# Kernel optimization log

Hardware: AMD Instinct MI355X
Metric: run time of the kernel (lower is better)

## Reference

```python
import jax, jax.numpy as jnp
import numpy as np

H = 256   # hidden_size
V = 47    # vocab
T = 257   # target sequence length (T-1 decode steps)
S = 1024  # encoder frames


def setup_inputs() -> dict:
    key = jax.random.key(0)
    ks = jax.random.split(key, 32)
    sc = 0.05
    n = lambda k, sh: jax.random.normal(k, sh, dtype=jnp.float32) * sc
    inp = {
        "Y": jax.random.randint(ks[0], (T,), 0, V),
        "h": n(ks[1], (3, 1, H)),
        "c": n(ks[2], (3, 1, H)),
        "outEncoder": n(ks[3], (S, H)),
        "emb": n(ks[4], (V, H)),
    }
    i = 5
    for l in (1, 2, 3):
        inp[f"W_ih{l}"] = n(ks[i], (4 * H, H)); i += 1
        inp[f"W_hh{l}"] = n(ks[i], (4 * H, H)); i += 1
        inp[f"b_ih{l}"] = n(ks[i], (4 * H,)); i += 1
        inp[f"b_hh{l}"] = n(ks[i], (4 * H,)); i += 1
    inp["att_vector"] = n(ks[i], (1, H)); i += 1
    inp["att_W"] = n(ks[i], (H, H)); i += 1
    inp["att_V"] = n(ks[i], (H, H)); i += 1
    inp["att_b"] = n(ks[i], (H, 1)); i += 1
    inp["mlp_w1"] = n(ks[i], (H, 2 * H)); i += 1
    inp["mlp_b1"] = n(ks[i], (H,)); i += 1
    inp["mlp_w2"] = n(ks[i], (H, H)); i += 1
    inp["mlp_b2"] = n(ks[i], (H,)); i += 1
    inp["mlp_w3"] = n(ks[i], (V, H)); i += 1
    inp["mlp_b3"] = n(ks[i], (V,)); i += 1
    inp["teacher_force"] = 0  # rand() > 0 always -> always teacher-forced (deterministic)
    return inp


def _lstm_cell(x, h, c, W_ih, W_hh, b_ih, b_hh):
    # PyTorch LSTMCell: gate order i, f, g, o
    g = x @ W_ih.T + b_ih + h @ W_hh.T + b_hh        # [1, 4H]
    i, f, gg, o = jnp.split(g, 4, axis=-1)
    c_new = jax.nn.sigmoid(f) * c + jax.nn.sigmoid(i) * jnp.tanh(gg)
    h_new = jax.nn.sigmoid(o) * jnp.tanh(c_new)
    return h_new, c_new


def reference(Y, h, c, outEncoder, emb,
              W_ih1, W_hh1, b_ih1, b_hh1,
              W_ih2, W_hh2, b_ih2, b_hh2,
              W_ih3, W_hh3, b_ih3, b_hh3,
              att_vector, att_W, att_V, att_b,
              mlp_w1, mlp_b1, mlp_w2, mlp_b2, mlp_w3, mlp_b3,
              teacher_force):
    # teacher_force == 0 -> ground-truth inputs every step (the only deterministic path)
    VOut = att_V @ outEncoder.T                      # [H, S], loop-invariant

    def step(carry, x):
        h0, c0, h1, c1, h2, c2 = carry
        h0, c0 = _lstm_cell(x, h0, c0, W_ih1, W_hh1, b_ih1, b_hh1)
        h1, c1 = _lstm_cell(h0, h1, c1, W_ih2, W_hh2, b_ih2, b_hh2)
        h2, c2 = _lstm_cell(h1, h2, c2, W_ih3, W_hh3, b_ih3, b_hh3)
        # Bahdanau-style attention: E = tanh(W h + V enc + b)
        WS = att_W @ h2.T                            # [H, 1] -> broadcasts over S
        E = jnp.tanh(WS + VOut + att_b)              # [H, S]
        e = att_vector @ E                           # [1, S]
        alpha = jax.nn.softmax(e, axis=1)            # [1, S]
        context = alpha @ outEncoder                 # [1, H]
        v = jnp.concatenate([h2, context], axis=1)   # [1, 2H]
        v = jax.nn.relu(v @ mlp_w1.T + mlp_b1)
        v = jax.nn.relu(v @ mlp_w2.T + mlp_b2)
        out = v @ mlp_w3.T + mlp_b3                  # [1, V]
        return (h0, c0, h1, c1, h2, c2), out

    xs = emb[Y[:-1]][:, None, :]                     # [T-1, 1, H] embedded teacher inputs
    init = (h[0], c[0], h[1], c[1], h[2], c[2])
    _, outs = jax.lax.scan(step, init, xs)
    return outs                                      # [T-1, 1, V]
```

## Files before the change

### kernel.cpp

```cpp
#include <hip/hip_runtime.h>


#define VOCAB  47
#define NSTEP  256
#define NREC   40
#define NTAIL  216
#define NMEGA  (NREC + NTAIL)

typedef unsigned long long u64;

#define F_H0A 64
#define F_H1A (F_H0A + 131584)
#define F_H2A (F_H1A + 131584)
#define F_X1  (F_H2A + 131584)
#define F_VB  (F_X1 + 262144)
#define F_W1T (F_VB + 262144)
#define F_W2T (F_W1T + 131072)
#define F_W3T (F_W2T + 65536)
#define F_AWT (F_W3T + 12032)

#define R_SHH 0
#define R_SHX 512
#define T_H2  0
#define T_WS  256
#define T_WSP 512
#define T_EX  1024
#define T_CAT 2048
#define T_O1  2560
#define T_O2  2816
#define T_AV  3072
#define T_RED 3328

__device__ __forceinline__ float fma4(float4 w, float4 h, float acc) {
    acc = fmaf(w.x, h.x, acc); acc = fmaf(w.y, h.y, acc);
    acc = fmaf(w.z, h.z, acc); acc = fmaf(w.w, h.w, acc);
    return acc;
}
__device__ __forceinline__ float sigm(float x) {
    return __builtin_amdgcn_rcpf(1.f + __expf(-x));
}
__device__ __forceinline__ float tanh_(float x) {
    float e = __expf(2.f * x);
    return 1.f - 2.f * __builtin_amdgcn_rcpf(e + 1.f);
}

__device__ __forceinline__ void tagstore(u64* p, float v, unsigned tag) {
    u64 pk = ((u64)tag << 32) | (u64)__float_as_uint(v);
    __hip_atomic_store(p, pk, __ATOMIC_RELAXED, __HIP_MEMORY_SCOPE_AGENT);
}
__device__ __forceinline__ float pollval(u64* p, unsigned tag) {
    u64 v;
    do { v = __hip_atomic_load(p, __ATOMIC_RELAXED, __HIP_MEMORY_SCOPE_AGENT); }
    while ((unsigned)(v >> 32) != tag);
    return __uint_as_float((unsigned)(v & 0xffffffffull));
}
__device__ __forceinline__ float pollval_slow(u64* p, unsigned tag) {
    u64 v;
    for (;;) {
        v = __hip_atomic_load(p, __ATOMIC_RELAXED, __HIP_MEMORY_SCOPE_AGENT);
        if ((unsigned)(v >> 32) == tag) break;
        __builtin_amdgcn_s_sleep(2);
    }
    return __uint_as_float((unsigned)(v & 0xffffffffull));
}

__global__ __launch_bounds__(256) void prep_kernel(
    const float* __restrict__ emb, const int* __restrict__ Y,
    const float* __restrict__ Wih1, const float* __restrict__ bih1,
    const float* __restrict__ bhh1,
    const float* __restrict__ enc, const float* __restrict__ attV,
    const float* __restrict__ attB,
    const float* __restrict__ w1, const float* __restrict__ w2,
    const float* __restrict__ w3, const float* __restrict__ attW,
    const float* __restrict__ h, float* __restrict__ wsf)
{
    __shared__ __align__(16) float psm[4160];
    const int id = blockIdx.x, tid = threadIdx.x;

    if (id < 512) {
        const float* Arows; const int* idx; const float* Brows;
        const float* bias1; const float* bias2; float* out; int C, rt, ct;
        if (id < 256) {
            Arows = emb; idx = Y; Brows = Wih1; bias1 = bih1; bias2 = bhh1;
            out = wsf + F_X1; C = 1024; rt = id & 15; ct = id >> 4;
        } else {
            Arows = enc; idx = nullptr; Brows = attV; bias1 = attB; bias2 = nullptr;
            out = wsf + F_VB; C = 256; rt = (id - 256) & 63; ct = (id - 256) >> 6;
        }
        float* sA = psm;
        const int rl = tid >> 4, l = tid & 15;
        const int r = rt * 16 + rl;
        const int cb = ct * 64;
        const int arow = idx ? idx[r] : r;
        const float* Ap = Arows + arow * 256;
#pragma unroll
        for (int q = 0; q < 4; ++q)
            *(float4*)(&sA[rl * 260 + l * 16 + 4 * q]) = *(const float4*)(Ap + l * 16 + 4 * q);
        __syncthreads();
        for (int cc = 0; cc < 64; ++cc) {
            const int c = cb + cc;
            const float* Bp = Brows + c * 256;
            float acc = 0.f;
#pragma unroll
            for (int q = 0; q < 4; ++q) {
                float4 b = *(const float4*)(Bp + l * 4 + 64 * q);
                float4 a = *(const float4*)(&sA[rl * 260 + l * 4 + 64 * q]);
                acc = fma4(b, a, acc);
            }
            acc += __shfl_xor(acc, 1); acc += __shfl_xor(acc, 2);
            acc += __shfl_xor(acc, 4); acc += __shfl_xor(acc, 8);
            if (l == 0) {
                float bb = bias1[c] + (bias2 ? bias2[c] : 0.f);
                out[(size_t)r * C + c] = acc + bb;
            }
        }
    } else if (id < 784) {
        const float* in; float* out; int rows, cols, bxi, byi;
        if (id < 640)      { in = w1;   out = wsf + F_W1T; rows = 256; cols = 512;
                             bxi = (id - 512) & 15; byi = (id - 512) >> 4; }
        else if (id < 704) { in = w2;   out = wsf + F_W2T; rows = 256; cols = 256;
                             bxi = (id - 640) & 7;  byi = (id - 640) >> 3; }
        else if (id < 720) { in = w3;   out = wsf + F_W3T; rows = VOCAB; cols = 256;
                             bxi = (id - 704) & 7;  byi = (id - 704) >> 3; }
        else               { in = attW; out = wsf + F_AWT; rows = 256; cols = 256;
                             bxi = (id - 720) & 7;  byi = (id - 720) >> 3; }
        float* tile = psm;
        const int tx = tid & 31, ty = tid >> 5;
        const int bx = bxi * 32, by = byi * 32;
        int x = bx + tx;
#pragma unroll
        for (int j = ty; j < 32; j += 8) {
            int y = by + j;
            if (x < cols && y < rows) tile[j * 33 + tx] = in[y * cols + x];
        }
        __syncthreads();
        x = by + tx;
#pragma unroll
        for (int j = ty; j < 32; j += 8) {
            int y = bx + j;
            if (x < rows && y < cols) out[y * rows + x] = tile[tx * 33 + j];
        }
    } else {
        tagstore((u64*)(wsf + F_H0A) + tid, h[tid],       1u);
        tagstore((u64*)(wsf + F_H1A) + tid, h[256 + tid], 1u);
        tagstore((u64*)(wsf + F_H2A) + tid, h[512 + tid], 1u);
    }
}

__global__ __launch_bounds__(512) void mega_kernel(
    const float* __restrict__ Whh1,
    const float* __restrict__ Wih2, const float* __restrict__ Whh2,
    const float* __restrict__ Wih3, const float* __restrict__ Whh3,
    const float* __restrict__ bih2, const float* __restrict__ bhh2,
    const float* __restrict__ bih3, const float* __restrict__ bhh3,
    const float* __restrict__ cin,  const float* __restrict__ av,
    const float* __restrict__ enc,
    const float* __restrict__ b1, const float* __restrict__ b2,
    const float* __restrict__ b3,
    float* __restrict__ wsf, float* __restrict__ out)
{
    __shared__ __align__(16) float smem[3456];
    const int tid = threadIdx.x, wg = blockIdx.x;
    const int wave = tid >> 6, wlane = tid & 63;

    u64* H0A = (u64*)(wsf + F_H0A);
    u64* H1A = (u64*)(wsf + F_H1A);
    u64* H2A = (u64*)(wsf + F_H2A);

    if (wg < 8) {
        const float* X1 = wsf + F_X1;
        const int ug = wlane >> 4, gate = (wlane >> 2) & 3, l4 = wlane & 3;
        const int u = wg * 32 + wave * 4 + ug;
        const int ju = gate * 256 + u;
        float4 wA[16];
        const float* wp = Whh1 + ju * 256;
#pragma unroll
        for (int m = 0; m < 16; ++m) wA[m] = *(const float4*)(wp + (m * 4 + l4) * 4);
        float creg = ((wlane & 15) == 0) ? cin[u] : 0.f;
        const int b16 = wlane & 48;

        float xv = (l4 == 0) ? X1[ju] : 0.f;
        for (int t = 0; t < NSTEP; ++t) {
            if (tid < 256)
                smem[R_SHH + (t & 1) * 256 + tid] = pollval(H0A + t * 256 + tid, t + 1);
            __syncthreads();
            const float4* a4 = (const float4*)(smem + R_SHH + (t & 1) * 256);
            float acc = xv;
#pragma unroll
            for (int m = 0; m < 16; ++m) acc = fma4(wA[m], a4[m * 4 + l4], acc);
            acc += __shfl_xor(acc, 1); acc += __shfl_xor(acc, 2);
            float gf = __shfl(acc, b16 + 4);
            float gg = __shfl(acc, b16 + 8);
            float go = __shfl(acc, b16 + 12);
            if ((wlane & 15) == 0) {
                float cn = sigm(gf) * creg + sigm(acc) * tanh_(gg);
                creg = cn;
                tagstore(H0A + (t + 1) * 256 + u, sigm(go) * tanh_(cn), t + 2);
            }
            if (t < NSTEP - 1) xv = (l4 == 0) ? X1[(t + 1) * 1024 + ju] : 0.f;
        }
    } else if (wg < NREC) {
        const int role = (wg < 24) ? 1 : 2;
        const int ug = wlane >> 5, gate = (wlane >> 3) & 3, l8 = wlane & 7;
        const int wgr = wg - (role == 1 ? 8 : 24);
        const int u = wgr * 16 + wave * 2 + ug;
        const int ju = gate * 256 + u;
        const float* Wi = (role == 1) ? Wih2 : Wih3;
        const float* Wh = (role == 1) ? Whh2 : Whh3;
        float4 wAi[8], wAh[8];
        const float* wip = Wi + ju * 256;
        const float* whp = Wh + ju * 256;
#pragma unroll
        for (int m = 0; m < 8; ++m) {
            wAi[m] = *(const float4*)(wip + (m * 8 + l8) * 4);
            wAh[m] = *(const float4*)(whp + (m * 8 + l8) * 4);
        }
        float biasr = (l8 == 0)
            ? ((role == 1) ? (bih2[ju] + bhh2[ju]) : (bih3[ju] + bhh3[ju])) : 0.f;
        float creg = ((wlane & 31) == 0) ? cin[((role == 1) ? 256 : 512) + u] : 0.f;
        u64* Hup  = (role == 1) ? H0A : H1A;
        u64* Hown = (role == 1) ? H1A : H2A;
        const int b32 = wlane & 32;

        if (tid < 256) smem[R_SHX + tid] = pollval(Hup + 256 + tid, 2);
        __syncthreads();
        float xacc;
        {
            const float4* x4 = (const float4*)(smem + R_SHX);
            float a = 0.f;
#pragma unroll
            for (int m = 0; m < 8; ++m) a = fma4(wAi[m], x4[m * 8 + l8], a);
            xacc = a;
        }

        for (int t = 0; t < NSTEP; ++t) {
            if (tid < 256)
                smem[R_SHH + (t & 1) * 256 + tid] = pollval(Hown + t * 256 + tid, t + 1);
            __syncthreads();
            const float4* h4 = (const float4*)(smem + R_SHH + (t & 1) * 256);
            float acc = xacc + biasr;
#pragma unroll
            for (int m = 0; m < 8; ++m) acc = fma4(wAh[m], h4[m * 8 + l8], acc);
            acc += __shfl_xor(acc, 1); acc += __shfl_xor(acc, 2); acc += __shfl_xor(acc, 4);
            float gf = __shfl(acc, b32 + 8);
            float gg = __shfl(acc, b32 + 16);
            float go = __shfl(acc, b32 + 24);
            if ((wlane & 31) == 0) {
                float cn = sigm(gf) * creg + sigm(acc) * tanh_(gg);
                creg = cn;
                tagstore(Hown + (t + 1) * 256 + u, sigm(go) * tanh_(cn), t + 2);
            }
            if (t < NSTEP - 1) {
                if (tid < 256)
                    smem[R_SHX + ((t + 1) & 1) * 256 + tid] =
                        pollval(Hup + (t + 2) * 256 + tid, t + 3);
                __syncthreads();
                const float4* x4 = (const float4*)(smem + R_SHX + ((t + 1) & 1) * 256);
                float a = 0.f;
#pragma unroll
                for (int m = 0; m < 8; ++m) a = fma4(wAi[m], x4[m * 8 + l8], a);
                xacc = a;
            }
        }
    } else {
        const float* VB  = wsf + F_VB;
        const float* W1T = wsf + F_W1T;
        const float* W2T = wsf + F_W2T;
        const float* W3T = wsf + F_W3T;
        const float* AWT = wsf + F_AWT;
        const int j = tid & 255, hf = tid >> 8;

        if (tid < 256) smem[T_AV + tid] = av[tid];

        for (int t = wg - NREC; t < NSTEP; t += NTAIL) {
            __syncthreads();
            if (tid < 256)
                smem[T_H2 + tid] = pollval_slow(H2A + (t + 1) * 256 + tid, t + 2);
            __syncthreads();
            {
                const float* wp = AWT + (size_t)(hf * 128) * 256 + j;
                const float* hp = smem + T_H2 + hf * 128;
                float p0 = 0.f, p1 = 0.f;
#pragma unroll 4
                for (int k = 0; k < 128; k += 2) {
                    p0 = fmaf(wp[k * 256], hp[k], p0);
                    p1 = fmaf(wp[(k + 1) * 256], hp[k + 1], p1);
                }
                smem[T_WSP + hf * 256 + j] = p0 + p1;
            }
            __syncthreads();
            if (tid < 256) smem[T_WS + tid] = smem[T_WSP + tid] + smem[T_WSP + 256 + tid];
            __syncthreads();
            {
                const float* avs_ = smem + T_AV;
                const float* ws_  = smem + T_WS;
#pragma unroll
                for (int rep = 0; rep < 2; ++rep) {
                    const int s = tid + rep * 512;
                    const float4* vb4 = (const float4*)(VB + (size_t)s * 256);
                    float e0 = 0.f, e1 = 0.f, e2 = 0.f, e3 = 0.f;
#pragma unroll 4
                    for (int q = 0; q < 64; ++q) {
                        float4 vb = vb4[q];
                        const int k = q * 4;
                        e0 = fmaf(avs_[k],     tanh_(ws_[k]     + vb.x), e0);
                        e1 = fmaf(avs_[k + 1], tanh_(ws_[k + 1] + vb.y), e1);
                        e2 = fmaf(avs_[k + 2], tanh_(ws_[k + 2] + vb.z), e2);
                        e3 = fmaf(avs_[k + 3], tanh_(ws_[k + 3] + vb.w), e3);
                    }
                    smem[T_EX + s] = __expf((e0 + e1) + (e2 + e3));
                }
            }
            __syncthreads();
            {
                float sv = smem[T_EX + tid] + smem[T_EX + 512 + tid];
                sv += __shfl_xor(sv, 1);  sv += __shfl_xor(sv, 2);
                sv += __shfl_xor(sv, 4);  sv += __shfl_xor(sv, 8);
                sv += __shfl_xor(sv, 16); sv += __shfl_xor(sv, 32);
                if (wlane == 0) smem[T_RED + wave] = sv;
            }
            __syncthreads();
            if (tid == 0) {
                float sm = 0.f;
#pragma unroll
                for (int i = 0; i < 8; ++i) sm += smem[T_RED + i];
                smem[T_RED + 8] = __builtin_amdgcn_rcpf(sm);
            }
            __syncthreads();
            {
                const float* ex_ = smem + T_EX + hf * 512;
                const float* ep  = enc + (size_t)(hf * 512) * 256 + j;
                float c0 = 0.f, c1 = 0.f, c2 = 0.f, c3 = 0.f;
#pragma unroll 2
                for (int s = 0; s < 512; s += 4) {
                    c0 = fmaf(ex_[s],     ep[(size_t)s * 256],       c0);
                    c1 = fmaf(ex_[s + 1], ep[(size_t)(s + 1) * 256], c1);
                    c2 = fmaf(ex_[s + 2], ep[(size_t)(s + 2) * 256], c2);
                    c3 = fmaf(ex_[s + 3], ep[(size_t)(s + 3) * 256], c3);
                }
                smem[T_WSP + hf * 256 + j] = (c0 + c1) + (c2 + c3);
            }
            __syncthreads();
            if (tid < 256) {
                smem[T_CAT + tid] = smem[T_H2 + tid];
                smem[T_CAT + 256 + tid] =
                    (smem[T_WSP + tid] + smem[T_WSP + 256 + tid]) * smem[T_RED + 8];
            }
            __syncthreads();
            {
                const float* wp = W1T + (size_t)(hf * 256) * 256 + j;
                const float* cp = smem + T_CAT + hf * 256;
                float p0 = 0.f, p1 = 0.f;
#pragma unroll 4
                for (int k = 0; k < 256; k += 2) {
                    p0 = fmaf(wp[(size_t)k * 256], cp[k], p0);
                    p1 = fmaf(wp[(size_t)(k + 1) * 256], cp[k + 1], p1);
                }
                smem[T_WSP + hf * 256 + j] = p0 + p1;
            }
            __syncthreads();
            if (tid < 256)
                smem[T_O1 + tid] =
                    fmaxf(b1[tid] + smem[T_WSP + tid] + smem[T_WSP + 256 + tid], 0.f);
            __syncthreads();
            {
                const float* wp = W2T + (size_t)(hf * 128) * 256 + j;
                const float* cp = smem + T_O1 + hf * 128;
                float p0 = 0.f, p1 = 0.f;
#pragma unroll 4
                for (int k = 0; k < 128; k += 2) {
                    p0 = fmaf(wp[(size_t)k * 256], cp[k], p0);
                    p1 = fmaf(wp[(size_t)(k + 1) * 256], cp[k + 1], p1);
                }
                smem[T_WSP + hf * 256 + j] = p0 + p1;
            }
            __syncthreads();
            if (tid < 256)
                smem[T_O2 + tid] =
                    fmaxf(b2[tid] + smem[T_WSP + tid] + smem[T_WSP + 256 + tid], 0.f);
            __syncthreads();
            if (tid < 8 * VOCAB) {
                const int jj = tid >> 3, l = tid & 7;
                const float* wp = W3T + (size_t)(l * 32) * VOCAB + jj;
                const float* vp = smem + T_O2 + l * 32;
                float p = 0.f;
#pragma unroll 4
                for (int k = 0; k < 32; ++k) p = fmaf(wp[(size_t)k * VOCAB], vp[k], p);
                p += __shfl_xor(p, 1); p += __shfl_xor(p, 2); p += __shfl_xor(p, 4);
                if (l == 0) out[t * VOCAB + jj] = b3[jj] + p;
            }
        }
    }
}

extern "C" void kernel_launch(void* const* d_in, const int* in_sizes, int n_in,
                              void* d_out, int out_size, void* d_ws, size_t ws_size,
                              hipStream_t stream)
{
    (void)in_sizes; (void)n_in; (void)out_size; (void)ws_size;
    const int*   Y    = (const int*)  d_in[0];
    const float* h    = (const float*)d_in[1];
    const float* c    = (const float*)d_in[2];
    const float* enc  = (const float*)d_in[3];
    const float* emb  = (const float*)d_in[4];
    const float* Wih1 = (const float*)d_in[5];
    const float* Whh1 = (const float*)d_in[6];
    const float* bih1 = (const float*)d_in[7];
    const float* bhh1 = (const float*)d_in[8];
    const float* Wih2 = (const float*)d_in[9];
    const float* Whh2 = (const float*)d_in[10];
    const float* bih2 = (const float*)d_in[11];
    const float* bhh2 = (const float*)d_in[12];
    const float* Wih3 = (const float*)d_in[13];
    const float* Whh3 = (const float*)d_in[14];
    const float* bih3 = (const float*)d_in[15];
    const float* bhh3 = (const float*)d_in[16];
    const float* av   = (const float*)d_in[17];
    const float* attW = (const float*)d_in[18];
    const float* attV = (const float*)d_in[19];
    const float* attB = (const float*)d_in[20];
    const float* w1   = (const float*)d_in[21];
    const float* b1   = (const float*)d_in[22];
    const float* w2   = (const float*)d_in[23];
    const float* b2   = (const float*)d_in[24];
    const float* w3   = (const float*)d_in[25];
    const float* b3   = (const float*)d_in[26];
    float* wsf = (float*)d_ws;
    float* out = (float*)d_out;

    prep_kernel<<<785, 256, 0, stream>>>(emb, Y, Wih1, bih1, bhh1,
                                         enc, attV, attB,
                                         w1, w2, w3, attW, h, wsf);

    mega_kernel<<<NMEGA, 512, 0, stream>>>(Whh1, Wih2, Whh2, Wih3, Whh3,
                                           bih2, bhh2, bih3, bhh3,
                                           c, av, enc, b1, b2, b3, wsf, out);
}
```

Measured before the change: 602.8 us.

## Split recurrent layers into input-projection and recurrence roles with ring buffers

Layers 2 and 3 are split into separate workgroup roles: one computes the input projection W_ih·h_{l-1} ahead of time into a 16-deep tagged ring buffer, and the other runs only the W_hh recurrence. The aim is to take the input GEMV off the serial recurrence path. Tail workgroups now wait on per-block progress counters with sleep, then read h2 with a tight poll. The prep work is split into two kernels: a transpose pass, then batched projections that use the transposed weights. In exchange the design needs more cross-workgroup synchronisation and a ring-buffer backpressure wait, which brings a risk of stalls or deadlock.

```diff
diff --git a/kernel.cpp b/kernel.cpp
--- a/kernel.cpp
+++ b/kernel.cpp
@@ -3,24 +3,28 @@
 
 #define VOCAB  47
 #define NSTEP  256
-#define NREC   40
-#define NTAIL  216
+#define NREC   20
+#define NTAIL  236
 #define NMEGA  (NREC + NTAIL)
 
 typedef unsigned long long u64;
 
-#define F_H0A 64
-#define F_H1A (F_H0A + 131584)
-#define F_H2A (F_H1A + 131584)
-#define F_X1  (F_H2A + 131584)
-#define F_VB  (F_X1 + 262144)
-#define F_W1T (F_VB + 262144)
-#define F_W2T (F_W1T + 131072)
-#define F_W3T (F_W2T + 65536)
-#define F_AWT (F_W3T + 12032)
-
-#define R_SHH 0
-#define R_SHX 512
+#define F_PROG  16
+#define F_H0A   64
+#define F_H1A   (F_H0A + 131584)
+#define F_H2A   (F_H1A + 131584)
+#define F_X1    (F_H2A + 131584)
+#define F_VB    (F_X1 + 262144)
+#define F_W1T   (F_VB + 262144)
+#define F_W2T   (F_W1T + 131072)
+#define F_W3T   (F_W2T + 65536)
+#define F_AWT   (F_W3T + 12032)
+#define F_OVL   (F_AWT + 65536)
+#define F_W1iT  F_OVL
+#define F_AVT   (F_OVL + 262144)
+#define F_G2X   F_OVL
+#define F_G3X   (F_OVL + 32768)
+
 #define T_H2  0
 #define T_WS  256
 #define T_WSP 512
@@ -43,7 +47,6 @@
     float e = __expf(2.f * x);
     return 1.f - 2.f * __builtin_amdgcn_rcpf(e + 1.f);
 }
-
 __device__ __forceinline__ void tagstore(u64* p, float v, unsigned tag) {
     u64 pk = ((u64)tag << 32) | (u64)__float_as_uint(v);
     __hip_atomic_store(p, pk, __ATOMIC_RELAXED, __HIP_MEMORY_SCOPE_AGENT);
@@ -54,100 +57,188 @@
     while ((unsigned)(v >> 32) != tag);
     return __uint_as_float((unsigned)(v & 0xffffffffull));
 }
-__device__ __forceinline__ float pollval_slow(u64* p, unsigned tag) {
-    u64 v;
-    for (;;) {
-        v = __hip_atomic_load(p, __ATOMIC_RELAXED, __HIP_MEMORY_SCOPE_AGENT);
-        if ((unsigned)(v >> 32) == tag) break;
-        __builtin_amdgcn_s_sleep(2);
-    }
-    return __uint_as_float((unsigned)(v & 0xffffffffull));
-}
-
-__global__ __launch_bounds__(256) void prep_kernel(
-    const float* __restrict__ emb, const int* __restrict__ Y,
-    const float* __restrict__ Wih1, const float* __restrict__ bih1,
-    const float* __restrict__ bhh1,
-    const float* __restrict__ enc, const float* __restrict__ attV,
-    const float* __restrict__ attB,
+
+__global__ __launch_bounds__(256) void prep0_kernel(
+    const float* __restrict__ Wih1, const float* __restrict__ attV,
     const float* __restrict__ w1, const float* __restrict__ w2,
     const float* __restrict__ w3, const float* __restrict__ attW,
     const float* __restrict__ h, float* __restrict__ wsf)
 {
-    __shared__ __align__(16) float psm[4160];
+    __shared__ float tile[32 * 33];
     const int id = blockIdx.x, tid = threadIdx.x;
-
-    if (id < 512) {
-        const float* Arows; const int* idx; const float* Brows;
-        const float* bias1; const float* bias2; float* out; int C, rt, ct;
-        if (id < 256) {
-            Arows = emb; idx = Y; Brows = Wih1; bias1 = bih1; bias2 = bhh1;
-            out = wsf + F_X1; C = 1024; rt = id & 15; ct = id >> 4;
-        } else {
-            Arows = enc; idx = nullptr; Brows = attV; bias1 = attB; bias2 = nullptr;
-            out = wsf + F_VB; C = 256; rt = (id - 256) & 63; ct = (id - 256) >> 6;
-        }
-        float* sA = psm;
-        const int rl = tid >> 4, l = tid & 15;
-        const int r = rt * 16 + rl;
-        const int cb = ct * 64;
-        const int arow = idx ? idx[r] : r;
-        const float* Ap = Arows + arow * 256;
-#pragma unroll
-        for (int q = 0; q < 4; ++q)
-            *(float4*)(&sA[rl * 260 + l * 16 + 4 * q]) = *(const float4*)(Ap + l * 16 + 4 * q);
-        __syncthreads();
-        for (int cc = 0; cc < 64; ++cc) {
-            const int c = cb + cc;
-            const float* Bp = Brows + c * 256;
-            float acc = 0.f;
-#pragma unroll
-            for (int q = 0; q < 4; ++q) {
-                float4 b = *(const float4*)(Bp + l * 4 + 64 * q);
-                float4 a = *(const float4*)(&sA[rl * 260 + l * 4 + 64 * q]);
-                acc = fma4(b, a, acc);
-            }
-            acc += __shfl_xor(acc, 1); acc += __shfl_xor(acc, 2);
-            acc += __shfl_xor(acc, 4); acc += __shfl_xor(acc, 8);
-            if (l == 0) {
-                float bb = bias1[c] + (bias2 ? bias2[c] : 0.f);
-                out[(size_t)r * C + c] = acc + bb;
-            }
-        }
-    } else if (id < 784) {
-        const float* in; float* out; int rows, cols, bxi, byi;
-        if (id < 640)      { in = w1;   out = wsf + F_W1T; rows = 256; cols = 512;
-                             bxi = (id - 512) & 15; byi = (id - 512) >> 4; }
-        else if (id < 704) { in = w2;   out = wsf + F_W2T; rows = 256; cols = 256;
-                             bxi = (id - 640) & 7;  byi = (id - 640) >> 3; }
-        else if (id < 720) { in = w3;   out = wsf + F_W3T; rows = VOCAB; cols = 256;
-                             bxi = (id - 704) & 7;  byi = (id - 704) >> 3; }
-        else               { in = attW; out = wsf + F_AWT; rows = 256; cols = 256;
-                             bxi = (id - 720) & 7;  byi = (id - 720) >> 3; }
-        float* tile = psm;
-        const int tx = tid & 31, ty = tid >> 5;
-        const int bx = bxi * 32, by = byi * 32;
-        int x = bx + tx;
-#pragma unroll
-        for (int j = ty; j < 32; j += 8) {
-            int y = by + j;
-            if (x < cols && y < rows) tile[j * 33 + tx] = in[y * cols + x];
-        }
-        __syncthreads();
-        x = by + tx;
-#pragma unroll
-        for (int j = ty; j < 32; j += 8) {
-            int y = bx + j;
-            if (x < rows && y < cols) out[y * rows + x] = tile[tx * 33 + j];
-        }
-    } else {
+    if (id == 592) {
         tagstore((u64*)(wsf + F_H0A) + tid, h[tid],       1u);
         tagstore((u64*)(wsf + F_H1A) + tid, h[256 + tid], 1u);
         tagstore((u64*)(wsf + F_H2A) + tid, h[512 + tid], 1u);
-    }
-}
-
-__global__ __launch_bounds__(512) void mega_kernel(
+        if (tid < 4) ((unsigned*)(wsf + F_PROG))[tid] = 1u;
+        return;
+    }
+    const float* in; float* out; int rows, cols, bxi, byi;
+    if (id < 256)      { in = Wih1; out = wsf + F_W1iT; rows = 1024; cols = 256; bxi = id & 7;          byi = id >> 3; }
+    else if (id < 320) { in = attV; out = wsf + F_AVT;  rows = 256;  cols = 256; bxi = (id - 256) & 7;  byi = (id - 256) >> 3; }
+    else if (id < 448) { in = w1;   out = wsf + F_W1T;  rows = 256;  cols = 512; bxi = (id - 320) & 15; byi = (id - 320) >> 4; }
+    else if (id < 512) { in = w2;   out = wsf + F_W2T;  rows = 256;  cols = 256; bxi = (id - 448) & 7;  byi = (id - 448) >> 3; }
+    else if (id < 528) { in = w3;   out = wsf + F_W3T;  rows = VOCAB;cols = 256; bxi = (id - 512) & 7;  byi = (id - 512) >> 3; }
+    else               { in = attW; out = wsf + F_AWT;  rows = 256;  cols = 256; bxi = (id - 528) & 7;  byi = (id - 528) >> 3; }
+    const int tx = tid & 31, ty = tid >> 5;
+    const int bx = bxi * 32, by = byi * 32;
+    int x = bx + tx;
+#pragma unroll
+    for (int jj = ty; jj < 32; jj += 8) {
+        int y = by + jj;
+        if (x < cols && y < rows) tile[jj * 33 + tx] = in[(size_t)y * cols + x];
+    }
+    __syncthreads();
+    x = by + tx;
+#pragma unroll
+    for (int jj = ty; jj < 32; jj += 8) {
+        int y = bx + jj;
+        if (x < rows && y < cols) out[(size_t)y * rows + x] = tile[tx * 33 + jj];
+    }
+}
+
+__global__ __launch_bounds__(256) void prep1_kernel(
+    const int* __restrict__ Y, const float* __restrict__ emb,
+    const float* __restrict__ bih1, const float* __restrict__ bhh1,
+    const float* __restrict__ enc, const float* __restrict__ attB,
+    float* __restrict__ wsf)
+{
+    __shared__ float As[8 * 256];
+    __shared__ int ys[8];
+    const int id = blockIdx.x, tid = threadIdx.x;
+    if (id < 32) {
+        const int t0 = id * 8;
+        if (tid < 8) ys[tid] = Y[t0 + tid];
+        __syncthreads();
+#pragma unroll
+        for (int q = 0; q < 8; ++q) As[q * 256 + tid] = emb[(size_t)ys[q] * 256 + tid];
+        __syncthreads();
+        const float* W1iT = wsf + F_W1iT;
+        float* X1 = wsf + F_X1;
+        for (int cch = 0; cch < 4; ++cch) {
+            const int j = cch * 256 + tid;
+            float bb = bih1[j] + bhh1[j];
+            float acc[8] = {0.f, 0.f, 0.f, 0.f, 0.f, 0.f, 0.f, 0.f};
+#pragma unroll 4
+            for (int k = 0; k < 256; ++k) {
+                float wv2 = W1iT[(size_t)k * 1024 + j];
+#pragma unroll
+                for (int q = 0; q < 8; ++q) acc[q] = fmaf(As[q * 256 + k], wv2, acc[q]);
+            }
+#pragma unroll
+            for (int q = 0; q < 8; ++q) X1[(size_t)(t0 + q) * 1024 + j] = acc[q] + bb;
+        }
+    } else {
+        const int s0 = (id - 32) * 8;
+#pragma unroll
+        for (int q = 0; q < 8; ++q) As[q * 256 + tid] = enc[(size_t)(s0 + q) * 256 + tid];
+        __syncthreads();
+        const float* AVT = wsf + F_AVT;
+        float* VB = wsf + F_VB;
+        float bb = attB[tid];
+        float acc[8] = {0.f, 0.f, 0.f, 0.f, 0.f, 0.f, 0.f, 0.f};
+#pragma unroll 4
+        for (int k = 0; k < 256; ++k) {
+            float wv2 = AVT[(size_t)k * 256 + tid];
+#pragma unroll
+            for (int q = 0; q < 8; ++q) acc[q] = fmaf(As[q * 256 + k], wv2, acc[q]);
+        }
+#pragma unroll
+        for (int q = 0; q < 8; ++q) VB[(size_t)(s0 + q) * 256 + tid] = acc[q] + bb;
+    }
+}
+
+__device__ __forceinline__ void role_h(
+    int w, const float* __restrict__ Whh, const float* __restrict__ cin,
+    const float* __restrict__ X1, u64* GX, u64* HPUB, unsigned* prog, float* hb)
+{
+    const int tid = threadIdx.x;
+    const int ul = tid >> 3, j = tid & 7, kh = j >> 2;
+    const int u = w * 64 + ul, row = (j & 3) * 256 + u;
+    float4 wv[32];
+    const float* wp = Whh + (size_t)row * 256 + kh * 128;
+#pragma unroll
+    for (int m = 0; m < 32; ++m) wv[m] = *(const float4*)(wp + 4 * m);
+    float creg = (j == 0) ? cin[u] : 0.f;
+    const int base = (tid & 63) & ~7;
+
+    for (int t = 0; t < NSTEP; ++t) {
+        if (tid < 256) hb[(t & 1) * 256 + tid] = pollval(HPUB + (size_t)t * 256 + tid, t + 1);
+        float xv = 0.f;
+        if (j < 4) xv = X1 ? X1[(size_t)t * 1024 + row]
+                           : pollval(GX + ((t & 15) * 1024 + row), t + 1);
+        __syncthreads();
+        const float4* h4 = (const float4*)(hb + (t & 1) * 256);
+        float a0 = 0.f, a1 = 0.f, a2 = 0.f, a3 = 0.f;
+#pragma unroll
+        for (int m = 0; m < 32; m += 4) {
+            a0 = fma4(wv[m],     h4[kh * 32 + m],     a0);
+            a1 = fma4(wv[m + 1], h4[kh * 32 + m + 1], a1);
+            a2 = fma4(wv[m + 2], h4[kh * 32 + m + 2], a2);
+            a3 = fma4(wv[m + 3], h4[kh * 32 + m + 3], a3);
+        }
+        float acc = (a0 + a1) + (a2 + a3);
+        acc += __shfl_xor(acc, 4);
+        acc += xv;
+        float gf = __shfl(acc, base + 1);
+        float gg = __shfl(acc, base + 2);
+        float go = __shfl(acc, base + 3);
+        if (j == 0) {
+            float cn = sigm(gf) * creg + sigm(acc) * tanh_(gg);
+            creg = cn;
+            tagstore(HPUB + (size_t)(t + 1) * 256 + u, sigm(go) * tanh_(cn), t + 2);
+        }
+        if (prog) {
+            asm volatile("s_waitcnt vmcnt(0)" ::: "memory");
+            __syncthreads();
+            if (tid == 0)
+                __hip_atomic_store(prog, (unsigned)(t + 2),
+                                   __ATOMIC_RELAXED, __HIP_MEMORY_SCOPE_AGENT);
+        }
+    }
+}
+
+__device__ __forceinline__ void role_x(
+    int w, const float* __restrict__ Wih, const float* __restrict__ bih,
+    const float* __restrict__ bhh, u64* HSRC, u64* GXD, u64* HCONS, float* hb)
+{
+    const int tid = threadIdx.x;
+    const int ul = tid >> 3, j = tid & 7, kh = j >> 2;
+    const int u = w * 64 + ul, row = (j & 3) * 256 + u;
+    float4 wv[32];
+    const float* wp = Wih + (size_t)row * 256 + kh * 128;
+#pragma unroll
+    for (int m = 0; m < 32; ++m) wv[m] = *(const float4*)(wp + 4 * m);
+    const float bias = bih[row] + bhh[row];
+
+    if (tid < 256) hb[tid] = pollval(HSRC + 256 + tid, 2);
+    __syncthreads();
+    for (int t = 0; t < NSTEP; ++t) {
+        float hn = 0.f;
+        if (t < NSTEP - 1 && tid < 256)
+            hn = pollval(HSRC + (size_t)(t + 2) * 256 + tid, t + 3);
+        const float4* h4 = (const float4*)(hb + (t & 1) * 256);
+        float a0 = 0.f, a1 = 0.f, a2 = 0.f, a3 = 0.f;
+#pragma unroll
+        for (int m = 0; m < 32; m += 4) {
+            a0 = fma4(wv[m],     h4[kh * 32 + m],     a0);
+            a1 = fma4(wv[m + 1], h4[kh * 32 + m + 1], a1);
+            a2 = fma4(wv[m + 2], h4[kh * 32 + m + 2], a2);
+            a3 = fma4(wv[m + 3], h4[kh * 32 + m + 3], a3);
+        }
+        float acc = (a0 + a1) + (a2 + a3);
+        acc += __shfl_xor(acc, 4);
+        if (j < 4) {
+            if (t >= 16)
+                pollval(HCONS + (size_t)(t - 15) * 256 + u, t - 14);
+            tagstore(GXD + ((t & 15) * 1024 + row), acc + bias, t + 1);
+        }
+        if (t < NSTEP - 1 && tid < 256) hb[((t + 1) & 1) * 256 + tid] = hn;
+        __syncthreads();
+    }
+}
+
+__global__ __launch_bounds__(512, 2) void mega_kernel(
     const float* __restrict__ Whh1,
     const float* __restrict__ Wih2, const float* __restrict__ Whh2,
     const float* __restrict__ Wih3, const float* __restrict__ Whh3,
@@ -166,102 +257,20 @@
     u64* H0A = (u64*)(wsf + F_H0A);
     u64* H1A = (u64*)(wsf + F_H1A);
     u64* H2A = (u64*)(wsf + F_H2A);
-
-    if (wg < 8) {
-        const float* X1 = wsf + F_X1;
-        const int ug = wlane >> 4, gate = (wlane >> 2) & 3, l4 = wlane & 3;
-        const int u = wg * 32 + wave * 4 + ug;
-        const int ju = gate * 256 + u;
-        float4 wA[16];
-        const float* wp = Whh1 + ju * 256;
-#pragma unroll
-        for (int m = 0; m < 16; ++m) wA[m] = *(const float4*)(wp + (m * 4 + l4) * 4);
-        float creg = ((wlane & 15) == 0) ? cin[u] : 0.f;
-        const int b16 = wlane & 48;
-
-        float xv = (l4 == 0) ? X1[ju] : 0.f;
-        for (int t = 0; t < NSTEP; ++t) {
-            if (tid < 256)
-                smem[R_SHH + (t & 1) * 256 + tid] = pollval(H0A + t * 256 + tid, t + 1);
-            __syncthreads();
-            const float4* a4 = (const float4*)(smem + R_SHH + (t & 1) * 256);
-            float acc = xv;
-#pragma unroll
-            for (int m = 0; m < 16; ++m) acc = fma4(wA[m], a4[m * 4 + l4], acc);
-            acc += __shfl_xor(acc, 1); acc += __shfl_xor(acc, 2);
-            float gf = __shfl(acc, b16 + 4);
-            float gg = __shfl(acc, b16 + 8);
-            float go = __shfl(acc, b16 + 12);
-            if ((wlane & 15) == 0) {
-                float cn = sigm(gf) * creg + sigm(acc) * tanh_(gg);
-                creg = cn;
-                tagstore(H0A + (t + 1) * 256 + u, sigm(go) * tanh_(cn), t + 2);
-            }
-            if (t < NSTEP - 1) xv = (l4 == 0) ? X1[(t + 1) * 1024 + ju] : 0.f;
-        }
+    u64* G2X = (u64*)(wsf + F_G2X);
+    u64* G3X = (u64*)(wsf + F_G3X);
+    unsigned* PROG = (unsigned*)(wsf + F_PROG);
+
+    if (wg < 4) {
+        role_h(wg, Whh1, cin, wsf + F_X1, nullptr, H0A, nullptr, smem);
+    } else if (wg < 8) {
+        role_x(wg - 4, Wih2, bih2, bhh2, H0A, G2X, H1A, smem);
+    } else if (wg < 12) {
+        role_h(wg - 8, Whh2, cin + 256, nullptr, G2X, H1A, nullptr, smem);
+    } else if (wg < 16) {
+        role_x(wg - 12, Wih3, bih3, bhh3, H1A, G3X, H2A, smem);
     } else if (wg < NREC) {
-        const int role = (wg < 24) ? 1 : 2;
-        const int ug = wlane >> 5, gate = (wlane >> 3) & 3, l8 = wlane & 7;
-        const int wgr = wg - (role == 1 ? 8 : 24);
-        const int u = wgr * 16 + wave * 2 + ug;
-        const int ju = gate * 256 + u;
-        const float* Wi = (role == 1) ? Wih2 : Wih3;
-        const float* Wh = (role == 1) ? Whh2 : Whh3;
-        float4 wAi[8], wAh[8];
-        const float* wip = Wi + ju * 256;
-        const float* whp = Wh + ju * 256;
-#pragma unroll
-        for (int m = 0; m < 8; ++m) {
-            wAi[m] = *(const float4*)(wip + (m * 8 + l8) * 4);
-            wAh[m] = *(const float4*)(whp + (m * 8 + l8) * 4);
-        }
-        float biasr = (l8 == 0)
-            ? ((role == 1) ? (bih2[ju] + bhh2[ju]) : (bih3[ju] + bhh3[ju])) : 0.f;
-        float creg = ((wlane & 31) == 0) ? cin[((role == 1) ? 256 : 512) + u] : 0.f;
-        u64* Hup  = (role == 1) ? H0A : H1A;
-        u64* Hown = (role == 1) ? H1A : H2A;
-        const int b32 = wlane & 32;
-
-        if (tid < 256) smem[R_SHX + tid] = pollval(Hup + 256 + tid, 2);
-        __syncthreads();
-        float xacc;
-        {
-            const float4* x4 = (const float4*)(smem + R_SHX);
-            float a = 0.f;
-#pragma unroll
-            for (int m = 0; m < 8; ++m) a = fma4(wAi[m], x4[m * 8 + l8], a);
-            xacc = a;
-        }
-
-        for (int t = 0; t < NSTEP; ++t) {
-            if (tid < 256)
-                smem[R_SHH + (t & 1) * 256 + tid] = pollval(Hown + t * 256 + tid, t + 1);
-            __syncthreads();
-            const float4* h4 = (const float4*)(smem + R_SHH + (t & 1) * 256);
-            float acc = xacc + biasr;
-#pragma unroll
-            for (int m = 0; m < 8; ++m) acc = fma4(wAh[m], h4[m * 8 + l8], acc);
-            acc += __shfl_xor(acc, 1); acc += __shfl_xor(acc, 2); acc += __shfl_xor(acc, 4);
-            float gf = __shfl(acc, b32 + 8);
-            float gg = __shfl(acc, b32 + 16);
-            float go = __shfl(acc, b32 + 24);
-            if ((wlane & 31) == 0) {
-                float cn = sigm(gf) * creg + sigm(acc) * tanh_(gg);
-                creg = cn;
-                tagstore(Hown + (t + 1) * 256 + u, sigm(go) * tanh_(cn), t + 2);
-            }
-            if (t < NSTEP - 1) {
-                if (tid < 256)
-                    smem[R_SHX + ((t + 1) & 1) * 256 + tid] =
-                        pollval(Hup + (t + 2) * 256 + tid, t + 3);
-                __syncthreads();
-                const float4* x4 = (const float4*)(smem + R_SHX + ((t + 1) & 1) * 256);
-                float a = 0.f;
-#pragma unroll
-                for (int m = 0; m < 8; ++m) a = fma4(wAi[m], x4[m * 8 + l8], a);
-                xacc = a;
-            }
-        }
+        role_h(wg - 16, Whh3, cin + 512, nullptr, G3X, H2A, PROG + (wg - 16), smem);
     } else {
         const float* VB  = wsf + F_VB;
         const float* W1T = wsf + F_W1T;
@@ -274,8 +283,15 @@
 
         for (int t = wg - NREC; t < NSTEP; t += NTAIL) {
             __syncthreads();
+            if (tid < 4) {
+                while (__hip_atomic_load(PROG + tid, __ATOMIC_RELAXED,
+                                         __HIP_MEMORY_SCOPE_AGENT) < (unsigned)(t + 2))
+                    __builtin_amdgcn_s_sleep(8);
+            }
+            asm volatile("" ::: "memory");
+            __syncthreads();
             if (tid < 256)
-                smem[T_H2 + tid] = pollval_slow(H2A + (t + 1) * 256 + tid, t + 2);
+                smem[T_H2 + tid] = pollval(H2A + (size_t)(t + 1) * 256 + tid, t + 2);
             __syncthreads();
             {
                 const float* wp = AWT + (size_t)(hf * 128) * 256 + j;
@@ -428,10 +444,8 @@
     float* wsf = (float*)d_ws;
     float* out = (float*)d_out;
 
-    prep_kernel<<<785, 256, 0, stream>>>(emb, Y, Wih1, bih1, bhh1,
-                                         enc, attV, attB,
-                                         w1, w2, w3, attW, h, wsf);
-
+    prep0_kernel<<<593, 256, 0, stream>>>(Wih1, attV, w1, w2, w3, attW, h, wsf);
+    prep1_kernel<<<160, 256, 0, stream>>>(Y, emb, bih1, bhh1, enc, attB, wsf);
     mega_kernel<<<NMEGA, 512, 0, stream>>>(Whh1, Wih2, Whh2, Wih3, Whh3,
                                            bih2, bhh2, bih3, bhh3,
                                            c, av, enc, b1, b2, b3, wsf, out);
```

Result: slower. 939.0 us (+55.8%).
